# Kernel optimization log

Measured on AMD Instinct MI355X. Metric: run time of the kernel, lower is better.

The kernel has to match this reference:

```python
import jax, jax.numpy as jnp
import numpy as np
from jax import lax

BATCH, SEQ = 2, 2048
D_MODEL = 1024
D_STATE = 16
D_CONV = 4
EXPAND = 2
VOCAB = 32000
D_INNER = EXPAND * D_MODEL          # 2048
DT_RANK = (D_MODEL + 15) // 16      # 64 (mamba-ssm default 'auto')
V2 = VOCAB + 2


def setup_inputs() -> dict:
    key = jax.random.key(0)
    ks = jax.random.split(key, 12)
    g = lambda k, shape, scale: (jax.random.normal(k, shape, jnp.float32) * scale)
    x = jax.random.randint(ks[0], (BATCH, SEQ), 0, V2, dtype=jnp.int64 if jax.config.jax_enable_x64 else jnp.int32)
    emb = g(ks[1], (V2, D_MODEL), 0.02)
    W_in = g(ks[2], (D_MODEL, 2 * D_INNER), D_MODEL ** -0.5)
    conv_w = g(ks[3], (D_INNER, D_CONV), 0.5)
    conv_b = jnp.zeros((D_INNER,), jnp.float32)
    W_x = g(ks[4], (D_INNER, DT_RANK + 2 * D_STATE), D_INNER ** -0.5)
    W_dt = g(ks[5], (DT_RANK, D_INNER), DT_RANK ** -0.5)
    b_dt = g(ks[6], (D_INNER,), 0.1) - 4.0  # small dt after softplus
    # S4D-real init: A_log = log(1..d_state) broadcast over d_inner
    A_log = jnp.log(jnp.broadcast_to(jnp.arange(1, D_STATE + 1, dtype=jnp.float32), (D_INNER, D_STATE)))
    D_skip = jnp.ones((D_INNER,), jnp.float32)
    W_out = g(ks[7], (D_INNER, D_MODEL), D_INNER ** -0.5)
    W_head = g(ks[8], (D_MODEL, V2), D_MODEL ** -0.5)
    b_head = jnp.zeros((V2,), jnp.float32)
    return {"x": x, "emb": emb, "W_in": W_in, "conv_w": conv_w, "conv_b": conv_b,
            "W_x": W_x, "W_dt": W_dt, "b_dt": b_dt, "A_log": A_log, "D_skip": D_skip,
            "W_out": W_out, "W_head": W_head, "b_head": b_head}


def _mamba_forward(tok_emb, W_in, conv_w, conv_b, W_x, W_dt, b_dt, A_log, D_skip, W_out):
    # tok_emb: [B, L, d_model]
    xz = tok_emb @ W_in                               # [B, L, 2*d_inner]
    xm, z = jnp.split(xz, [D_INNER], axis=-1)
    # causal depthwise conv1d over time
    xc = lax.conv_general_dilated(
        xm.transpose(0, 2, 1),                        # [B, d_inner, L]
        conv_w[:, None, :],                           # [d_inner, 1, d_conv]
        window_strides=(1,), padding=[(D_CONV - 1, 0)],
        dimension_numbers=("NCH", "OIH", "NCH"),
        feature_group_count=D_INNER)
    xc = jax.nn.silu((xc + conv_b[None, :, None]).transpose(0, 2, 1))  # [B, L, d_inner]
    dbl = xc @ W_x                                    # [B, L, dt_rank + 2*d_state]
    dt_r, B_ssm, C_ssm = jnp.split(dbl, [DT_RANK, DT_RANK + D_STATE], axis=-1)
    dt = jax.nn.softplus(dt_r @ W_dt + b_dt)          # [B, L, d_inner]
    A = -jnp.exp(A_log)                               # [d_inner, d_state]

    def step(h, inp):
        dt_t, B_t, C_t, x_t = inp                     # [B,D],[B,N],[B,N],[B,D]
        dA = jnp.exp(dt_t[:, :, None] * A)            # [B, D, N]
        h = dA * h + (dt_t * x_t)[:, :, None] * B_t[:, None, :]
        y = jnp.einsum("bdn,bn->bd", h, C_t)
        return h, y

    h0 = jnp.zeros((tok_emb.shape[0], D_INNER, D_STATE), tok_emb.dtype)
    xs = (dt.transpose(1, 0, 2), B_ssm.transpose(1, 0, 2),
          C_ssm.transpose(1, 0, 2), xc.transpose(1, 0, 2))
    _, ys = lax.scan(step, h0, xs)                    # ys: [L, B, d_inner]
    y = ys.transpose(1, 0, 2) + xc * D_skip
    y = y * jax.nn.silu(z)
    return y @ W_out                                  # [B, L, d_model]


def reference(x, emb, W_in, conv_w, conv_b, W_x, W_dt, b_dt, A_log, D_skip, W_out, W_head, b_head):
    tok = emb[x]                                      # [B, L, d_model]
    m_out = _mamba_forward(tok, W_in, conv_w, conv_b, W_x, W_dt, b_dt, A_log, D_skip, W_out)
    logits = m_out @ W_head + b_head                  # [B, L, V+2]
    return logits.transpose(0, 2, 1)                  # pred_logits: [B, V+2, L]
```

## Files before the change

kernel.cpp:

```cpp
#include <hip/hip_runtime.h>
#include <cstddef>
#include <cstdint>


typedef __bf16 bf16x8 __attribute__((ext_vector_type(8)));
typedef float f32x4 __attribute__((ext_vector_type(4)));

__device__ __forceinline__ float sigmoidf_(float x) {
  return 1.0f / (1.0f + __expf(-x));
}

__device__ __forceinline__ unsigned short f2bf(float v) {
  unsigned u = __float_as_uint(v);
  u += 0x7fffu + ((u >> 16) & 1u);
  return (unsigned short)(u >> 16);
}
__device__ __forceinline__ float bf2f(unsigned short h) {
  return __uint_as_float(((unsigned)h) << 16);
}

__device__ __forceinline__ void gload_lds16(const void* g, void* l) {
  typedef const unsigned int GQ __attribute__((address_space(1)));
  typedef unsigned int LQ __attribute__((address_space(3)));
  __builtin_amdgcn_global_load_lds((GQ*)(unsigned long long)g,
                                   (LQ*)(unsigned)(unsigned long long)l,
                                   16, 0, 0);
}

__global__ __launch_bounds__(256) void split_wT_kernel(
    const float* __restrict__ W, int Nreal, unsigned short* __restrict__ hi,
    unsigned short* __restrict__ lo, int K) {
  __shared__ float tile[64][65];
  const int k0 = blockIdx.x * 64, n0 = blockIdx.y * 64;
  const int tq = threadIdx.x >> 6;
  const int tl = threadIdx.x & 63;
#pragma unroll
  for (int r = 0; r < 16; ++r) {
    int kk = r * 4 + tq;
    int n = n0 + tl;
    tile[kk][tl] = (n < Nreal) ? W[(size_t)(k0 + kk) * Nreal + n] : 0.f;
  }
  __syncthreads();
#pragma unroll
  for (int r = 0; r < 16; ++r) {
    int nn = r * 4 + tq;
    int n = n0 + nn;
    int k = k0 + tl;
    float v = tile[tl][nn];
    unsigned short h = f2bf(v);
    unsigned short l = f2bf(v - bf2f(h));
    int key = (n >> 1) & 3;
    size_t o = (size_t)n * K + (size_t)(k & ~31) +
               (size_t)(((((k >> 3) & 3) ^ key)) << 3) + (size_t)(k & 7);
    hi[o] = h;
    lo[o] = l;
  }
}

__global__ __launch_bounds__(256) void tok_split_kernel(
    const int* __restrict__ x, const float* __restrict__ emb,
    unsigned short* __restrict__ th, unsigned short* __restrict__ tlo) {
  const int i = blockIdx.x * 256 + threadIdx.x;
  const int t = i >> 7;
  const int sb = i & 127;
  const int row = x[t];
  const float* src = emb + (size_t)row * 1024 + (size_t)sb * 8;
  float4 v0 = *(const float4*)(src);
  float4 v1 = *(const float4*)(src + 4);
  float vv[8] = {v0.x, v0.y, v0.z, v0.w, v1.x, v1.y, v1.z, v1.w};
  unsigned hu[4], lu[4];
#pragma unroll
  for (int j = 0; j < 4; ++j) {
    unsigned short h0 = f2bf(vv[2 * j]), h1 = f2bf(vv[2 * j + 1]);
    unsigned short l0 = f2bf(vv[2 * j] - bf2f(h0));
    unsigned short l1 = f2bf(vv[2 * j + 1] - bf2f(h1));
    hu[j] = (unsigned)h0 | ((unsigned)h1 << 16);
    lu[j] = (unsigned)l0 | ((unsigned)l1 << 16);
  }
  const int key = (t >> 1) & 3;
  const int sdst = (sb & 3) ^ key;
  size_t o = (size_t)t * 1024 + (size_t)(sb >> 2) * 32 + (size_t)sdst * 8;
  *(uint4*)(th + o) = make_uint4(hu[0], hu[1], hu[2], hu[3]);
  *(uint4*)(tlo + o) = make_uint4(lu[0], lu[1], lu[2], lu[3]);
}

__global__ __launch_bounds__(256) void split_mo_kernel(
    const float* __restrict__ mo, unsigned short* __restrict__ mhi,
    unsigned short* __restrict__ mlo) {
  const int i = blockIdx.x * 256 + threadIdx.x;
  const int t = i >> 7;
  const int sb = i & 127;
  const float* src = mo + (size_t)t * 1024 + (size_t)sb * 8;
  float4 v0 = *(const float4*)(src);
  float4 v1 = *(const float4*)(src + 4);
  float vv[8] = {v0.x, v0.y, v0.z, v0.w, v1.x, v1.y, v1.z, v1.w};
  unsigned hu[4], lu[4];
#pragma unroll
  for (int j = 0; j < 4; ++j) {
    unsigned short h0 = f2bf(vv[2 * j]), h1 = f2bf(vv[2 * j + 1]);
    unsigned short l0 = f2bf(vv[2 * j] - bf2f(h0));
    unsigned short l1 = f2bf(vv[2 * j + 1] - bf2f(h1));
    hu[j] = (unsigned)h0 | ((unsigned)h1 << 16);
    lu[j] = (unsigned)l0 | ((unsigned)l1 << 16);
  }
  const int key = (t >> 1) & 3;
  const int sdst = (sb & 3) ^ key;
  size_t o = (size_t)t * 1024 + (size_t)(sb >> 2) * 32 + (size_t)sdst * 8;
  *(uint4*)(mhi + o) = make_uint4(hu[0], hu[1], hu[2], hu[3]);
  *(uint4*)(mlo + o) = make_uint4(lu[0], lu[1], lu[2], lu[3]);
}

template <int K, int OUTMODE, int BT>
__global__ __launch_bounds__(256, 2) void gemm_mfma_kernel(
    const unsigned short* __restrict__ Ah_, const unsigned short* __restrict__ Al_,
    const unsigned short* __restrict__ Bh_, const unsigned short* __restrict__ Bl_,
    const float* __restrict__ bias, float* __restrict__ out, int ldo) {
  __shared__ unsigned short Ah[4096], Al[4096], Bh[4096], Bl[4096];
  const int tid = threadIdx.x;
  const int lane = tid & 63, wid = tid >> 6;
  const int wr = wid >> 1, wc = wid & 1;
  const int chunk = (int)gridDim.x >> 3;
  const int swz = ((blockIdx.x & 7) * chunk) + (blockIdx.x >> 3);
  const int R0 = (swz / BT) * 128;
  const int C0 = (swz % BT) * 128;

  const int c0 = tid, c1 = tid + 256;
  const int r0 = c0 >> 2, s0 = (c0 & 3) * 8;
  const int r1 = c1 >> 2, s1 = (c1 & 3) * 8;
  const unsigned short* pA0h = Ah_ + (size_t)(R0 + r0) * K + s0;
  const unsigned short* pA0l = Al_ + (size_t)(R0 + r0) * K + s0;
  const unsigned short* pB0h = Bh_ + (size_t)(C0 + r0) * K + s0;
  const unsigned short* pB0l = Bl_ + (size_t)(C0 + r0) * K + s0;
  const unsigned short* pA1h = Ah_ + (size_t)(R0 + r1) * K + s1;
  const unsigned short* pA1l = Al_ + (size_t)(R0 + r1) * K + s1;
  const unsigned short* pB1h = Bh_ + (size_t)(C0 + r1) * K + s1;
  const unsigned short* pB1l = Bl_ + (size_t)(C0 + r1) * K + s1;
  unsigned short* lA0 = Ah + c0 * 8;
  unsigned short* lA1 = Ah + c1 * 8;
  unsigned short* lAl0 = Al + c0 * 8;
  unsigned short* lAl1 = Al + c1 * 8;
  unsigned short* lB0 = Bh + c0 * 8;
  unsigned short* lB1 = Bh + c1 * 8;
  unsigned short* lBl0 = Bl + c0 * 8;
  unsigned short* lBl1 = Bl + c1 * 8;

#define STAGE_T(KOFF)                 \
  do {                                \
    gload_lds16(pA0h + (KOFF), lA0);  \
    gload_lds16(pA1h + (KOFF), lA1);  \
    gload_lds16(pA0l + (KOFF), lAl0); \
    gload_lds16(pA1l + (KOFF), lAl1); \
    gload_lds16(pB0h + (KOFF), lB0);  \
    gload_lds16(pB1h + (KOFF), lB1);  \
    gload_lds16(pB0l + (KOFF), lBl0); \
    gload_lds16(pB1l + (KOFF), lBl1); \
  } while (0)

  const int fr = lane & 15;
  const int kb = (lane >> 4) * 8;
  int aoff[4], boff[4];
#pragma unroll
  for (int m = 0; m < 4; ++m) {
    int r = 64 * wr + 16 * m + fr;
    aoff[m] = r * 32 + (kb ^ (((r >> 1) & 3) << 3));
  }
#pragma unroll
  for (int nf = 0; nf < 4; ++nf) {
    int r = 64 * wc + 16 * nf + fr;
    boff[nf] = r * 32 + (kb ^ (((r >> 1) & 3) << 3));
  }

  f32x4 acc[4][4];
#pragma unroll
  for (int m = 0; m < 4; ++m)
#pragma unroll
    for (int nf = 0; nf < 4; ++nf) acc[m][nf] = f32x4{0.f, 0.f, 0.f, 0.f};

  STAGE_T(0);
  int koff = 32;
  constexpr int KSTEPS = K / 32;
  for (int ks = 0; ks < KSTEPS; ++ks) {
    __syncthreads();
    bf16x8 ah[4], al[4], bh[4], bl[4];
#pragma unroll
    for (int m = 0; m < 4; ++m) {
      ah[m] = *(const bf16x8*)(Ah + aoff[m]);
      al[m] = *(const bf16x8*)(Al + aoff[m]);
    }
#pragma unroll
    for (int nf = 0; nf < 4; ++nf) {
      bh[nf] = *(const bf16x8*)(Bh + boff[nf]);
      bl[nf] = *(const bf16x8*)(Bl + boff[nf]);
    }
    __syncthreads();
    if (ks < KSTEPS - 1) {
      STAGE_T(koff);
      koff += 32;
    }
#pragma unroll
    for (int m = 0; m < 4; ++m)
#pragma unroll
      for (int nf = 0; nf < 4; ++nf) {
        acc[m][nf] = __builtin_amdgcn_mfma_f32_16x16x32_bf16(
            ah[m], bh[nf], acc[m][nf], 0, 0, 0);
        acc[m][nf] = __builtin_amdgcn_mfma_f32_16x16x32_bf16(
            ah[m], bl[nf], acc[m][nf], 0, 0, 0);
        acc[m][nf] = __builtin_amdgcn_mfma_f32_16x16x32_bf16(
            al[m], bh[nf], acc[m][nf], 0, 0, 0);
      }
  }
#undef STAGE_T

  const int frow = 4 * (lane >> 4);
#pragma unroll
  for (int m = 0; m < 4; ++m) {
    const int gr_base = R0 + 64 * wr + 16 * m + frow;
#pragma unroll
    for (int r = 0; r < 4; ++r) {
      const int gr = gr_base + r;
      if constexpr (OUTMODE == 1) {
        if (gr < 32002) {
          const float bb = bias[gr];
#pragma unroll
          for (int nf = 0; nf < 4; ++nf) {
            const int gc = C0 + 64 * wc + 16 * nf + fr;
            const int b_idx = gc >> 11;
            const int l = gc & 2047;
            out[((size_t)b_idx * 32002 + gr) * 2048 + l] = acc[m][nf][r] + bb;
          }
        }
      } else {
#pragma unroll
        for (int nf = 0; nf < 4; ++nf) {
          const int gc = C0 + 64 * wc + 16 * nf + fr;
          out[(size_t)gr * ldo + gc] = acc[m][nf][r];
        }
      }
    }
  }
}

__global__ __launch_bounds__(256) void conv_silu_kernel(
    const float* __restrict__ xz, const float* __restrict__ conv_w,
    const float* __restrict__ conv_b, float* __restrict__ xc) {
  const int idx = blockIdx.x * 256 + threadIdx.x;
  const int t = idx >> 11, d = idx & 2047;
  const int l = t & 2047;
  const float4 w = *(const float4*)(conv_w + (size_t)d * 4);
  const float ww[4] = {w.x, w.y, w.z, w.w};
  float s = conv_b[d];
  const float* xm = xz + d;
#pragma unroll
  for (int j = 0; j < 4; ++j) {
    int lj = l - 3 + j;
    if (lj >= 0) s = fmaf(ww[j], xm[(size_t)(t - 3 + j) * 4096], s);
  }
  xc[idx] = s * sigmoidf_(s);
}

__global__ __launch_bounds__(256) void gemm_dbl_kernel(
    const float* __restrict__ xc, const float* __restrict__ Wx,
    float* __restrict__ dbl) {
  const int idx = blockIdx.x * 256 + threadIdx.x;
  const int tq = idx / 96, c = idx % 96;
  const size_t t0 = (size_t)tq * 4;
  const float* a0 = xc + t0 * 2048;
  float acc[4] = {0.f, 0.f, 0.f, 0.f};
  for (int k = 0; k < 2048; k += 4) {
    float w0 = Wx[(size_t)(k + 0) * 96 + c];
    float w1 = Wx[(size_t)(k + 1) * 96 + c];
    float w2 = Wx[(size_t)(k + 2) * 96 + c];
    float w3 = Wx[(size_t)(k + 3) * 96 + c];
#pragma unroll
    for (int i = 0; i < 4; ++i) {
      float4 avv = *(const float4*)(a0 + (size_t)i * 2048 + k);
      acc[i] = fmaf(avv.x, w0, acc[i]);
      acc[i] = fmaf(avv.y, w1, acc[i]);
      acc[i] = fmaf(avv.z, w2, acc[i]);
      acc[i] = fmaf(avv.w, w3, acc[i]);
    }
  }
#pragma unroll
  for (int i = 0; i < 4; ++i) dbl[(t0 + i) * 96 + c] = acc[i];
}

__global__ __launch_bounds__(256) void gemm_dt_kernel(
    const float* __restrict__ dbl, const float* __restrict__ Wdt,
    const float* __restrict__ b_dt, float* __restrict__ dt) {
  __shared__ float s[4][64];
  const int t0 = (blockIdx.x >> 3) * 4;
  const int d = ((blockIdx.x & 7) << 8) + threadIdx.x;
  {
    int tt = threadIdx.x >> 6, k = threadIdx.x & 63;
    s[tt][k] = dbl[(size_t)(t0 + tt) * 96 + k];
  }
  __syncthreads();
  const float bd = b_dt[d];
  float acc[4] = {bd, bd, bd, bd};
#pragma unroll 16
  for (int k = 0; k < 64; ++k) {
    float w = Wdt[(size_t)k * 2048 + d];
#pragma unroll
    for (int i = 0; i < 4; ++i) acc[i] = fmaf(s[i][k], w, acc[i]);
  }
#pragma unroll
  for (int i = 0; i < 4; ++i) {
    float v = acc[i];
    float sp = (v > 20.f) ? v : log1pf(__expf(v));
    dt[(size_t)(t0 + i) * 2048 + d] = sp;
  }
}

__global__ __launch_bounds__(256) void scan_kernel(
    const float* __restrict__ dt, const float* __restrict__ xc,
    const float* __restrict__ dbl, const float* __restrict__ A_log,
    float* __restrict__ y) {
  const int tid = threadIdx.x;
  const int n = tid & 15;
  const int dloc = tid >> 4;
  const int b = blockIdx.x >> 7;
  const int d = ((blockIdx.x & 127) << 4) + dloc;
  const float A = -__expf(A_log[(size_t)d * 16 + n]);
  float h = 0.f;
  const size_t tb = (size_t)b * 2048;
  const float* dtp = dt + tb * 2048 + d;
  const float* xcp = xc + tb * 2048 + d;
  const float* Bp = dbl + tb * 96 + 64 + n;
  const float* Cp = dbl + tb * 96 + 80 + n;
  float* yo = y + tb * 2048 + d;

  constexpr int CH = 8;
  float cdt[CH], cx[CH], cB[CH], cC[CH];
#pragma unroll
  for (int j = 0; j < CH; ++j) {
    cdt[j] = dtp[(size_t)j * 2048];
    cx[j] = xcp[(size_t)j * 2048];
    cB[j] = Bp[(size_t)j * 96];
    cC[j] = Cp[(size_t)j * 96];
  }
  for (int t0 = 0; t0 < 2048; t0 += CH) {
    float ndt[CH], nx[CH], nB[CH], nC[CH];
    const bool more = (t0 + CH < 2048);
    if (more) {
#pragma unroll
      for (int j = 0; j < CH; ++j) {
        size_t o = (size_t)(t0 + CH + j);
        ndt[j] = dtp[o * 2048];
        nx[j] = xcp[o * 2048];
        nB[j] = Bp[o * 96];
        nC[j] = Cp[o * 96];
      }
    }
#pragma unroll
    for (int j = 0; j < CH; ++j) {
      float dA = __expf(cdt[j] * A);
      h = fmaf(dA, h, cdt[j] * cx[j] * cB[j]);
      float p = h * cC[j];
      p += __shfl_xor(p, 1);
      p += __shfl_xor(p, 2);
      p += __shfl_xor(p, 4);
      p += __shfl_xor(p, 8);
      if (n == 0) yo[(size_t)(t0 + j) * 2048] = p;
    }
    if (more) {
#pragma unroll
      for (int j = 0; j < CH; ++j) {
        cdt[j] = ndt[j]; cx[j] = nx[j]; cB[j] = nB[j]; cC[j] = nC[j];
      }
    }
  }
}

__global__ __launch_bounds__(256) void ypost_split_kernel(
    const float* __restrict__ y, const float* __restrict__ xc,
    const float* __restrict__ xz, const float* __restrict__ Dskip,
    unsigned short* __restrict__ yh, unsigned short* __restrict__ yl) {
  const size_t idx = ((size_t)blockIdx.x * 256 + threadIdx.x) * 4;
  const size_t t = idx >> 11;
  const int d = (int)(idx & 2047);
  float4 yv = *(const float4*)(y + idx);
  float4 xv = *(const float4*)(xc + idx);
  float4 zv = *(const float4*)(xz + t * 4096 + 2048 + d);
  float4 Dv = *(const float4*)(Dskip + d);
  float yy[4] = {yv.x, yv.y, yv.z, yv.w};
  float xx[4] = {xv.x, xv.y, xv.z, xv.w};
  float zz[4] = {zv.x, zv.y, zv.z, zv.w};
  float dd[4] = {Dv.x, Dv.y, Dv.z, Dv.w};
  unsigned short hs[4], ls[4];
#pragma unroll
  for (int i = 0; i < 4; ++i) {
    float t1 = fmaf(xx[i], dd[i], yy[i]);
    float r = t1 * (zz[i] * sigmoidf_(zz[i]));
    unsigned short h = f2bf(r);
    hs[i] = h;
    ls[i] = f2bf(r - bf2f(h));
  }
  const int key = ((int)t >> 1) & 3;
  const size_t o = t * 2048 + (size_t)(d & ~31) +
                   (size_t)((((d >> 3) & 3) ^ key) << 3) + (size_t)(d & 7);
  *(ushort4*)(yh + o) = make_ushort4(hs[0], hs[1], hs[2], hs[3]);
  *(ushort4*)(yl + o) = make_ushort4(ls[0], ls[1], ls[2], ls[3]);
}

extern "C" void kernel_launch(void* const* d_in, const int* in_sizes, int n_in,
                              void* d_out, int out_size, void* d_ws,
                              size_t ws_size, hipStream_t stream) {
  const int* x = (const int*)d_in[0];
  const float* emb = (const float*)d_in[1];
  const float* W_in = (const float*)d_in[2];
  const float* conv_w = (const float*)d_in[3];
  const float* conv_b = (const float*)d_in[4];
  const float* W_x = (const float*)d_in[5];
  const float* W_dt = (const float*)d_in[6];
  const float* b_dt = (const float*)d_in[7];
  const float* A_log = (const float*)d_in[8];
  const float* D_skip = (const float*)d_in[9];
  const float* W_out = (const float*)d_in[10];
  const float* W_head = (const float*)d_in[11];
  const float* b_head = (const float*)d_in[12];
  float* out = (float*)d_out;

  float* ws = (float*)d_ws;
  float* xz = ws;
  float* xc = ws + 16777216;
  float* dbl = ws + 25165824;
  float* dt = ws + 25559040;
  float* y = ws + 33947648;
  float* mo = ws + 42336256;
  unsigned short* tokh = (unsigned short*)(ws + 33947648);
  unsigned short* tokl = (unsigned short*)(ws + 36044800);
  unsigned short* WiTh = (unsigned short*)(ws + 38141952);
  unsigned short* WiTl = (unsigned short*)(ws + 40239104);
  unsigned short* yh = (unsigned short*)(ws + 25165824);
  unsigned short* yl = (unsigned short*)(ws + 29360128);
  unsigned short* WoTh = (unsigned short*)(ws + 0);
  unsigned short* WoTl = (unsigned short*)(ws + 1048576);
  unsigned short* Wt_hi = (unsigned short*)(ws + 0);
  unsigned short* Wt_lo = (unsigned short*)(ws + 16449536);
  unsigned short* mo_hi = (unsigned short*)(ws + 32899072);
  unsigned short* mo_lo = (unsigned short*)(ws + 34996224);

  dim3 blk(256);
  tok_split_kernel<<<2048, blk, 0, stream>>>(x, emb, tokh, tokl);
  split_wT_kernel<<<dim3(16, 64), blk, 0, stream>>>(W_in, 4096, WiTh, WiTl, 1024);
  gemm_mfma_kernel<1024, 0, 32><<<1024, blk, 0, stream>>>(
      tokh, tokl, WiTh, WiTl, nullptr, xz, 4096);
  conv_silu_kernel<<<32768, blk, 0, stream>>>(xz, conv_w, conv_b, xc);
  gemm_dbl_kernel<<<384, blk, 0, stream>>>(xc, W_x, dbl);
  gemm_dt_kernel<<<8192, blk, 0, stream>>>(dbl, W_dt, b_dt, dt);
  scan_kernel<<<256, blk, 0, stream>>>(dt, xc, dbl, A_log, y);
  ypost_split_kernel<<<8192, blk, 0, stream>>>(y, xc, xz, D_skip, yh, yl);
  split_wT_kernel<<<dim3(32, 16), blk, 0, stream>>>(W_out, 1024, WoTh, WoTl, 2048);
  gemm_mfma_kernel<2048, 0, 8><<<256, blk, 0, stream>>>(
      yh, yl, WoTh, WoTl, nullptr, mo, 1024);
  split_wT_kernel<<<dim3(16, 502), blk, 0, stream>>>(W_head, 32002, Wt_hi, Wt_lo, 1024);
  split_mo_kernel<<<2048, blk, 0, stream>>>(mo, mo_hi, mo_lo);
  gemm_mfma_kernel<1024, 1, 32><<<8032, blk, 0, stream>>>(
      Wt_hi, Wt_lo, mo_hi, mo_lo, b_head, out, 2048);
}
```

Before: 2.333 ms.

## Add 256x256 double-buffered MFMA GEMM and chunk-parallel selective scan

New measurement: 2.071 ms. -11.3%, faster.

```diff
diff --git a/kernel.cpp b/kernel.cpp
--- a/kernel.cpp
+++ b/kernel.cpp
@@ -25,6 +25,10 @@
   __builtin_amdgcn_global_load_lds((GQ*)(unsigned long long)g,
                                    (LQ*)(unsigned)(unsigned long long)l,
                                    16, 0, 0);
+}
+
+__device__ __forceinline__ f32x4 mfma16(bf16x8 a, bf16x8 b, f32x4 c) {
+  return __builtin_amdgcn_mfma_f32_16x16x32_bf16(a, b, c, 0, 0, 0);
 }
 
 __global__ __launch_bounds__(256) void split_wT_kernel(
@@ -108,6 +112,130 @@
   size_t o = (size_t)t * 1024 + (size_t)(sb >> 2) * 32 + (size_t)sdst * 8;
   *(uint4*)(mhi + o) = make_uint4(hu[0], hu[1], hu[2], hu[3]);
   *(uint4*)(mlo + o) = make_uint4(lu[0], lu[1], lu[2], lu[3]);
+}
+
+template <int K, int OUTMODE, int CT>
+__global__ __launch_bounds__(512, 2) void gemm256_kernel(
+    const unsigned short* __restrict__ Ah_, const unsigned short* __restrict__ Al_,
+    const unsigned short* __restrict__ Bh_, const unsigned short* __restrict__ Bl_,
+    const float* __restrict__ bias, float* __restrict__ out, int ldo) {
+  __shared__ unsigned short sAh[2][8192], sAl[2][8192];
+  __shared__ unsigned short sBh[2][8192], sBl[2][8192];
+  const int tid = threadIdx.x;
+  const int lane = tid & 63, wid = tid >> 6;
+  const int wr = wid >> 2, wc = wid & 3;
+  const int chunk = (int)gridDim.x >> 3;
+  const int swz = ((blockIdx.x & 7) * chunk) + (blockIdx.x >> 3);
+  const int R0 = (swz / CT) * 256;
+  const int C0 = (swz % CT) * 256;
+
+  const int rr = tid >> 2, ss = (tid & 3) * 8;
+  const unsigned short* gAh0 = Ah_ + (size_t)(R0 + rr) * K + ss;
+  const unsigned short* gAl0 = Al_ + (size_t)(R0 + rr) * K + ss;
+  const unsigned short* gBh0 = Bh_ + (size_t)(C0 + rr) * K + ss;
+  const unsigned short* gBl0 = Bl_ + (size_t)(C0 + rr) * K + ss;
+  const unsigned short* gAh1 = gAh0 + (size_t)128 * K;
+  const unsigned short* gAl1 = gAl0 + (size_t)128 * K;
+  const unsigned short* gBh1 = gBh0 + (size_t)128 * K;
+  const unsigned short* gBl1 = gBl0 + (size_t)128 * K;
+  const int l0 = tid * 8, l1 = tid * 8 + 4096;
+
+#define STAGE256(BUF, KOFF)                      \
+  do {                                           \
+    gload_lds16(gAh0 + (KOFF), &sAh[BUF][l0]);   \
+    gload_lds16(gAh1 + (KOFF), &sAh[BUF][l1]);   \
+    gload_lds16(gAl0 + (KOFF), &sAl[BUF][l0]);   \
+    gload_lds16(gAl1 + (KOFF), &sAl[BUF][l1]);   \
+    gload_lds16(gBh0 + (KOFF), &sBh[BUF][l0]);   \
+    gload_lds16(gBh1 + (KOFF), &sBh[BUF][l1]);   \
+    gload_lds16(gBl0 + (KOFF), &sBl[BUF][l0]);   \
+    gload_lds16(gBl1 + (KOFF), &sBl[BUF][l1]);   \
+  } while (0)
+
+  const int fr = lane & 15;
+  const int kb = (lane >> 4) * 8;
+  int aoff[8], boff[4];
+#pragma unroll
+  for (int m = 0; m < 8; ++m) {
+    int r = 128 * wr + 16 * m + fr;
+    aoff[m] = r * 32 + (kb ^ (((r >> 1) & 3) << 3));
+  }
+#pragma unroll
+  for (int nf = 0; nf < 4; ++nf) {
+    int r = 64 * wc + 16 * nf + fr;
+    boff[nf] = r * 32 + (kb ^ (((r >> 1) & 3) << 3));
+  }
+
+  f32x4 acc[8][4];
+#pragma unroll
+  for (int m = 0; m < 8; ++m)
+#pragma unroll
+    for (int nf = 0; nf < 4; ++nf) acc[m][nf] = f32x4{0.f, 0.f, 0.f, 0.f};
+
+  STAGE256(0, 0);
+  constexpr int KSTEPS = K / 32;
+  for (int ks = 0; ks < KSTEPS; ++ks) {
+    const int cur = ks & 1;
+    __syncthreads();
+    bf16x8 bh[4], bl[4];
+#pragma unroll
+    for (int p = 0; p < 4; ++p) {
+      bf16x8 a0h = *(const bf16x8*)&sAh[cur][aoff[2 * p]];
+      bf16x8 a0l = *(const bf16x8*)&sAl[cur][aoff[2 * p]];
+      bf16x8 a1h = *(const bf16x8*)&sAh[cur][aoff[2 * p + 1]];
+      bf16x8 a1l = *(const bf16x8*)&sAl[cur][aoff[2 * p + 1]];
+      if (p == 0) {
+#pragma unroll
+        for (int nf = 0; nf < 4; ++nf) {
+          bh[nf] = *(const bf16x8*)&sBh[cur][boff[nf]];
+          bl[nf] = *(const bf16x8*)&sBl[cur][boff[nf]];
+        }
+        if (ks + 1 < KSTEPS) STAGE256(cur ^ 1, (ks + 1) * 32);
+      }
+      __builtin_amdgcn_s_barrier();
+      __builtin_amdgcn_s_setprio(1);
+#pragma unroll
+      for (int nf = 0; nf < 4; ++nf) {
+        acc[2 * p][nf] = mfma16(a0h, bh[nf], acc[2 * p][nf]);
+        acc[2 * p][nf] = mfma16(a0h, bl[nf], acc[2 * p][nf]);
+        acc[2 * p][nf] = mfma16(a0l, bh[nf], acc[2 * p][nf]);
+        acc[2 * p + 1][nf] = mfma16(a1h, bh[nf], acc[2 * p + 1][nf]);
+        acc[2 * p + 1][nf] = mfma16(a1h, bl[nf], acc[2 * p + 1][nf]);
+        acc[2 * p + 1][nf] = mfma16(a1l, bh[nf], acc[2 * p + 1][nf]);
+      }
+      __builtin_amdgcn_s_setprio(0);
+      __builtin_amdgcn_s_barrier();
+    }
+  }
+#undef STAGE256
+
+  const int frow = 4 * (lane >> 4);
+#pragma unroll
+  for (int m = 0; m < 8; ++m) {
+    const int gr_base = R0 + 128 * wr + 16 * m + frow;
+#pragma unroll
+    for (int r = 0; r < 4; ++r) {
+      const int gr = gr_base + r;
+      if constexpr (OUTMODE == 1) {
+        if (gr < 32002) {
+          const float bb = bias[gr];
+#pragma unroll
+          for (int nf = 0; nf < 4; ++nf) {
+            const int gc = C0 + 64 * wc + 16 * nf + fr;
+            const int b_idx = gc >> 11;
+            const int l = gc & 2047;
+            out[((size_t)b_idx * 32002 + gr) * 2048 + l] = acc[m][nf][r] + bb;
+          }
+        }
+      } else {
+#pragma unroll
+        for (int nf = 0; nf < 4; ++nf) {
+          const int gc = C0 + 64 * wc + 16 * nf + fr;
+          out[(size_t)gr * ldo + gc] = acc[m][nf][r];
+        }
+      }
+    }
+  }
 }
 
 template <int K, int OUTMODE, int BT>
@@ -201,12 +329,9 @@
     for (int m = 0; m < 4; ++m)
 #pragma unroll
       for (int nf = 0; nf < 4; ++nf) {
-        acc[m][nf] = __builtin_amdgcn_mfma_f32_16x16x32_bf16(
-            ah[m], bh[nf], acc[m][nf], 0, 0, 0);
-        acc[m][nf] = __builtin_amdgcn_mfma_f32_16x16x32_bf16(
-            ah[m], bl[nf], acc[m][nf], 0, 0, 0);
-        acc[m][nf] = __builtin_amdgcn_mfma_f32_16x16x32_bf16(
-            al[m], bh[nf], acc[m][nf], 0, 0, 0);
+        acc[m][nf] = mfma16(ah[m], bh[nf], acc[m][nf]);
+        acc[m][nf] = mfma16(ah[m], bl[nf], acc[m][nf]);
+        acc[m][nf] = mfma16(al[m], bh[nf], acc[m][nf]);
       }
   }
 #undef STAGE_T
@@ -311,23 +436,25 @@
   }
 }
 
-__global__ __launch_bounds__(256) void scan_kernel(
+__global__ __launch_bounds__(256) void scan_local_kernel(
     const float* __restrict__ dt, const float* __restrict__ xc,
     const float* __restrict__ dbl, const float* __restrict__ A_log,
-    float* __restrict__ y) {
+    float* __restrict__ y, float* __restrict__ hend, float* __restrict__ send) {
   const int tid = threadIdx.x;
   const int n = tid & 15;
   const int dloc = tid >> 4;
-  const int b = blockIdx.x >> 7;
-  const int d = ((blockIdx.x & 127) << 4) + dloc;
+  const int c = blockIdx.x & 7;
+  const int dg = (blockIdx.x >> 3) & 127;
+  const int b = blockIdx.x >> 10;
+  const int d = dg * 16 + dloc;
   const float A = -__expf(A_log[(size_t)d * 16 + n]);
-  float h = 0.f;
-  const size_t tb = (size_t)b * 2048;
-  const float* dtp = dt + tb * 2048 + d;
-  const float* xcp = xc + tb * 2048 + d;
-  const float* Bp = dbl + tb * 96 + 64 + n;
-  const float* Cp = dbl + tb * 96 + 80 + n;
-  float* yo = y + tb * 2048 + d;
+  float h = 0.f, sdt = 0.f;
+  const size_t trow = (size_t)b * 2048 + (size_t)c * 256;
+  const float* dtp = dt + trow * 2048 + d;
+  const float* xcp = xc + trow * 2048 + d;
+  const float* Bp = dbl + trow * 96 + 64 + n;
+  const float* Cp = dbl + trow * 96 + 80 + n;
+  float* yo = y + trow * 2048 + d;
 
   constexpr int CH = 8;
   float cdt[CH], cx[CH], cB[CH], cC[CH];
@@ -338,9 +465,9 @@
     cB[j] = Bp[(size_t)j * 96];
     cC[j] = Cp[(size_t)j * 96];
   }
-  for (int t0 = 0; t0 < 2048; t0 += CH) {
+  for (int t0 = 0; t0 < 256; t0 += CH) {
     float ndt[CH], nx[CH], nB[CH], nC[CH];
-    const bool more = (t0 + CH < 2048);
+    const bool more = (t0 + CH < 256);
     if (more) {
 #pragma unroll
       for (int j = 0; j < CH; ++j) {
@@ -355,6 +482,7 @@
     for (int j = 0; j < CH; ++j) {
       float dA = __expf(cdt[j] * A);
       h = fmaf(dA, h, cdt[j] * cx[j] * cB[j]);
+      sdt += cdt[j];
       float p = h * cC[j];
       p += __shfl_xor(p, 1);
       p += __shfl_xor(p, 2);
@@ -366,6 +494,69 @@
 #pragma unroll
       for (int j = 0; j < CH; ++j) {
         cdt[j] = ndt[j]; cx[j] = nx[j]; cB[j] = nB[j]; cC[j] = nC[j];
+      }
+    }
+  }
+  hend[(((size_t)b * 8 + c) * 2048 + d) * 16 + n] = h;
+  if (n == 0) send[((size_t)b * 8 + c) * 2048 + d] = sdt;
+}
+
+__global__ __launch_bounds__(256) void scan_fix_kernel(
+    const float* __restrict__ dt, const float* __restrict__ dbl,
+    const float* __restrict__ A_log, const float* __restrict__ hend,
+    const float* __restrict__ send, float* __restrict__ y) {
+  const int c = blockIdx.x & 7;
+  if (c == 0) return;
+  const int tid = threadIdx.x;
+  const int n = tid & 15;
+  const int dloc = tid >> 4;
+  const int dg = (blockIdx.x >> 3) & 127;
+  const int b = blockIdx.x >> 10;
+  const int d = dg * 16 + dloc;
+  const float A = -__expf(A_log[(size_t)d * 16 + n]);
+  float G = 0.f;
+  for (int cp = 0; cp < c; ++cp) {
+    float P = __expf(A * send[((size_t)b * 8 + cp) * 2048 + d]);
+    G = fmaf(P, G, hend[(((size_t)b * 8 + cp) * 2048 + d) * 16 + n]);
+  }
+  const size_t trow = (size_t)b * 2048 + (size_t)c * 256;
+  const float* dtp = dt + trow * 2048 + d;
+  const float* Cp = dbl + trow * 96 + 80 + n;
+  float* yo = y + trow * 2048 + d;
+  float cum = 0.f;
+
+  constexpr int CH = 8;
+  float cdt[CH], cC[CH];
+#pragma unroll
+  for (int j = 0; j < CH; ++j) {
+    cdt[j] = dtp[(size_t)j * 2048];
+    cC[j] = Cp[(size_t)j * 96];
+  }
+  for (int t0 = 0; t0 < 256; t0 += CH) {
+    float ndt[CH], nC[CH];
+    const bool more = (t0 + CH < 256);
+    if (more) {
+#pragma unroll
+      for (int j = 0; j < CH; ++j) {
+        size_t o = (size_t)(t0 + CH + j);
+        ndt[j] = dtp[o * 2048];
+        nC[j] = Cp[o * 96];
+      }
+    }
+#pragma unroll
+    for (int j = 0; j < CH; ++j) {
+      cum += cdt[j];
+      float p = __expf(A * cum) * G * cC[j];
+      p += __shfl_xor(p, 1);
+      p += __shfl_xor(p, 2);
+      p += __shfl_xor(p, 4);
+      p += __shfl_xor(p, 8);
+      if (n == 0) yo[(size_t)(t0 + j) * 2048] += p;
+    }
+    if (more) {
+#pragma unroll
+      for (int j = 0; j < CH; ++j) {
+        cdt[j] = ndt[j]; cC[j] = nC[j];
       }
     }
   }
@@ -431,30 +622,34 @@
   unsigned short* tokl = (unsigned short*)(ws + 36044800);
   unsigned short* WiTh = (unsigned short*)(ws + 38141952);
   unsigned short* WiTl = (unsigned short*)(ws + 40239104);
+  float* hend = ws + 42336256;
+  float* send = ws + 42860544;
   unsigned short* yh = (unsigned short*)(ws + 25165824);
   unsigned short* yl = (unsigned short*)(ws + 29360128);
   unsigned short* WoTh = (unsigned short*)(ws + 0);
   unsigned short* WoTl = (unsigned short*)(ws + 1048576);
   unsigned short* Wt_hi = (unsigned short*)(ws + 0);
-  unsigned short* Wt_lo = (unsigned short*)(ws + 16449536);
-  unsigned short* mo_hi = (unsigned short*)(ws + 32899072);
-  unsigned short* mo_lo = (unsigned short*)(ws + 34996224);
+  unsigned short* Wt_lo = (unsigned short*)(ws + 16515072);
+  unsigned short* mo_hi = (unsigned short*)(ws + 33554432);
+  unsigned short* mo_lo = (unsigned short*)(ws + 35651584);
 
   dim3 blk(256);
+  dim3 blk512(512);
   tok_split_kernel<<<2048, blk, 0, stream>>>(x, emb, tokh, tokl);
   split_wT_kernel<<<dim3(16, 64), blk, 0, stream>>>(W_in, 4096, WiTh, WiTl, 1024);
-  gemm_mfma_kernel<1024, 0, 32><<<1024, blk, 0, stream>>>(
+  gemm256_kernel<1024, 0, 16><<<256, blk512, 0, stream>>>(
       tokh, tokl, WiTh, WiTl, nullptr, xz, 4096);
   conv_silu_kernel<<<32768, blk, 0, stream>>>(xz, conv_w, conv_b, xc);
   gemm_dbl_kernel<<<384, blk, 0, stream>>>(xc, W_x, dbl);
   gemm_dt_kernel<<<8192, blk, 0, stream>>>(dbl, W_dt, b_dt, dt);
-  scan_kernel<<<256, blk, 0, stream>>>(dt, xc, dbl, A_log, y);
+  scan_local_kernel<<<2048, blk, 0, stream>>>(dt, xc, dbl, A_log, y, hend, send);
+  scan_fix_kernel<<<2048, blk, 0, stream>>>(dt, dbl, A_log, hend, send, y);
   ypost_split_kernel<<<8192, blk, 0, stream>>>(y, xc, xz, D_skip, yh, yl);
   split_wT_kernel<<<dim3(32, 16), blk, 0, stream>>>(W_out, 1024, WoTh, WoTl, 2048);
   gemm_mfma_kernel<2048, 0, 8><<<256, blk, 0, stream>>>(
       yh, yl, WoTh, WoTl, nullptr, mo, 1024);
-  split_wT_kernel<<<dim3(16, 502), blk, 0, stream>>>(W_head, 32002, Wt_hi, Wt_lo, 1024);
+  split_wT_kernel<<<dim3(16, 504), blk, 0, stream>>>(W_head, 32002, Wt_hi, Wt_lo, 1024);
   split_mo_kernel<<<2048, blk, 0, stream>>>(mo, mo_hi, mo_lo);
-  gemm_mfma_kernel<1024, 1, 32><<<8032, blk, 0, stream>>>(
+  gemm256_kernel<1024, 1, 16><<<2016, blk512, 0, stream>>>(
       Wt_hi, Wt_lo, mo_hi, mo_lo, b_head, out, 2048);
 }
```
